# Kernel optimization log

Measured on AMD Instinct MI355X. Metric: run time of the kernel, lower is better.

## Reference

```python
import jax, jax.numpy as jnp
import numpy as np

N = 50000   # full-order mesh size
n = 10      # latent dim
MU = 32     # neighbourhood / window size
B = 8       # batch of snapshots


def setup_inputs() -> dict:
    key = jax.random.key(0)
    ks = jax.random.split(key, 6)
    x = jax.random.normal(ks[0], (B, N), jnp.float32)
    enc_w = jax.random.normal(ks[1], (n, N), jnp.float32) * 0.01  # torch Linear weight [n, N]
    enc_b = jax.random.normal(ks[2], (n,), jnp.float32) * 0.01
    decoder = jax.random.uniform(ks[3], (n, N), jnp.float32, minval=-0.01, maxval=0.01)
    bandwidth_layers = jax.random.uniform(ks[4], (n, n, N), jnp.float32, minval=-0.01, maxval=0.01)
    neighbours = jax.random.randint(ks[5], (N, MU), 0, N, jnp.int32)
    return dict(x=x, enc_w=enc_w, enc_b=enc_b, decoder=decoder,
                bandwidth_layers=bandwidth_layers, neighbours=neighbours)


def reference(x, enc_w, enc_b, decoder, bandwidth_layers, neighbours):
    mu = neighbours.shape[1]
    # encode: torch Linear -> x @ W.T + b                      [B, n]
    encoded = x @ enc_w.T + enc_b
    # bandwidths: bmm(encoded.repeat(n,1,1), bw).permute(1,0,2) -> sigmoid   [B, n, N]
    w = jax.nn.sigmoid(jnp.einsum('bk,ikp->bip', encoded, bandwidth_layers))
    # bubble window per scalar w: relu(1 - x^2/(w*mu)^2), normalized over mu  [B, n, N, mu]
    xs2 = (jnp.arange(mu, dtype=x.dtype) ** 2)  # [mu]
    win = jax.nn.relu(1.0 - xs2 / (w[..., None] * mu) ** 2)
    win = win / jnp.sum(win, axis=-1, keepdims=True)
    # gather decoder rows at each node's neighbours            [n, N, mu]
    gathered = jnp.take(decoder, neighbours, axis=1)
    # smooth_vec: sum over neighbourhood                       [B, n, N]
    smoothed = jnp.einsum('ipm,bipm->bip', gathered, win)
    # final bmm: encoded [B,1,n] @ smoothed [B,n,N] -> [B,N]
    return jnp.einsum('bi,bip->bp', encoded, smoothed)
```

## Files before the change

kernel.cpp:

```cpp
#include <hip/hip_runtime.h>
#include <hip/hip_bf16.h>

#define N_NODES 50000
#define NLAT 10
#define MU 32
#define BATCH 8
#define CHUNK 2000
#define NCHUNK 25
#define ENC_BLOCKS (BATCH * NLAT * NCHUNK)
#define TR_BLOCKS ((N_NODES + 255) / 256)
#define DT_STRIDE 16
#define NPB 64

typedef float v2f __attribute__((ext_vector_type(2)));

static __device__ __forceinline__ v2f v2_fma(v2f a, v2f b, v2f c) {
#if __has_builtin(__builtin_elementwise_fma)
    return __builtin_elementwise_fma(a, b, c);
#else
    v2f r; r[0] = fmaf(a[0], b[0], c[0]); r[1] = fmaf(a[1], b[1], c[1]); return r;
#endif
}
static __device__ __forceinline__ v2f v2_max0(v2f a) {
#if __has_builtin(__builtin_elementwise_max)
    v2f z = {0.0f, 0.0f};
    return __builtin_elementwise_max(a, z);
#else
    v2f r; r[0] = fmaxf(a[0], 0.0f); r[1] = fmaxf(a[1], 0.0f); return r;
#endif
}

__global__ __launch_bounds__(256) void encode_a_transpose(
    const float* __restrict__ x, const float* __restrict__ enc_w,
    const float* __restrict__ dec,
    float* __restrict__ partial, float* __restrict__ dec_t) {
    const int bid = blockIdx.x;
    if (bid < ENC_BLOCKS) {
        const int c  = bid % NCHUNK;
        const int bi = bid / NCHUNK;
        const int b = bi / NLAT, i = bi % NLAT;
        const float4* xr = (const float4*)(x + (size_t)b * N_NODES + c * CHUNK);
        const float4* wr = (const float4*)(enc_w + (size_t)i * N_NODES + c * CHUNK);
        float part = 0.0f;
        for (int q = threadIdx.x; q < CHUNK / 4; q += 256) {
            float4 xv = xr[q], wv = wr[q];
            part += xv.x * wv.x + xv.y * wv.y + xv.z * wv.z + xv.w * wv.w;
        }
        for (int off = 32; off; off >>= 1) part += __shfl_down(part, off, 64);
        __shared__ float s[4];
        if ((threadIdx.x & 63) == 0) s[threadIdx.x >> 6] = part;
        __syncthreads();
        if (threadIdx.x == 0) partial[bid] = (s[0] + s[1]) + (s[2] + s[3]);
    } else {
        const int p = (bid - ENC_BLOCKS) * 256 + threadIdx.x;
        if (p >= N_NODES) return;
        float v[DT_STRIDE];
        #pragma unroll
        for (int i = 0; i < NLAT; ++i) v[i] = dec[(size_t)i * N_NODES + p];
        #pragma unroll
        for (int i = NLAT; i < DT_STRIDE; ++i) v[i] = 0.0f;
        float4* dst = (float4*)(dec_t + (size_t)p * DT_STRIDE);
        #pragma unroll
        for (int q = 0; q < 4; ++q)
            dst[q] = make_float4(v[4*q], v[4*q+1], v[4*q+2], v[4*q+3]);
    }
}

__global__ __launch_bounds__(512) void nrbs_main_kernel(
    const float* __restrict__ dec_t,
    const float* __restrict__ bw,
    const int*   __restrict__ nbr,
    const float* __restrict__ partial,
    const float* __restrict__ enc_b,
    float*       __restrict__ out) {
    __shared__ float s_enc[BATCH * NLAT];
    __shared__ float s_inv[NLAT][NPB][BATCH];
    __shared__ int   s_tm[NPB];
    __shared__ int   s_nbr[NPB][MU + 1];
    const int tid   = threadIdx.x;
    const int node0 = blockIdx.x * NPB;

    if (tid < BATCH * NLAT) {
        float s = 0.0f;
        #pragma unroll
        for (int c = 0; c < NCHUNK; ++c) s += partial[tid * NCHUNK + c];
        s_enc[tid] = s + enc_b[tid % NLAT];
    }
    if (tid < NPB) s_tm[tid] = 0;
    {
        const int node = tid >> 3, ch = tid & 7;
        int4 v = make_int4(0, 0, 0, 0);
        if (node0 + node < N_NODES)
            v = ((const int4*)(nbr + (size_t)(node0 + node) * MU))[ch];
        s_nbr[node][ch * 4 + 0] = v.x; s_nbr[node][ch * 4 + 1] = v.y;
        s_nbr[node][ch * 4 + 2] = v.z; s_nbr[node][ch * 4 + 3] = v.w;
    }
    __syncthreads();

    {
        const int g    = tid >> 6;
        const int lane = tid & 63;
        const int p    = node0 + lane;
        if (p < N_NODES) {
            float tloc = 0.0f;
            for (int i = g; i < NLAT; i += 8) {
                float bwv[NLAT];
                #pragma unroll
                for (int k = 0; k < NLAT; ++k)
                    bwv[k] = bw[((size_t)(i * NLAT + k)) * N_NODES + p];
                float invv[BATCH];
                #pragma unroll
                for (int b = 0; b < BATCH; ++b) {
                    float z = 0.0f;
                    #pragma unroll
                    for (int k = 0; k < NLAT; ++k)
                        z = fmaf(s_enc[b * NLAT + k], bwv[k], z);
                    const float sg = 1.0f / (1.0f + __expf(-z));
                    const float t  = sg * (float)MU;
                    tloc = fmaxf(tloc, t);
                    invv[b] = __builtin_amdgcn_rcpf(t * t);
                }
                float4* dst = (float4*)&s_inv[i][lane][0];
                dst[0] = make_float4(invv[0], invv[1], invv[2], invv[3]);
                dst[1] = make_float4(invv[4], invv[5], invv[6], invv[7]);
            }
            atomicMax(&s_tm[lane], __float_as_int(tloc));
        }
    }
    __syncthreads();

    const int node  = tid >> 3;
    const int ipair = tid & 7;
    const int p     = node0 + node;
    const int i0    = 2 * ipair;
    const bool act  = (ipair < 5) && (p < N_NODES);

    v2f inv2[2][4], asum[2][4], ssum[2][4];
    #pragma unroll
    for (int ii = 0; ii < 2; ++ii)
        #pragma unroll
        for (int b2 = 0; b2 < 4; ++b2) {
            inv2[ii][b2] = (v2f){0.0f, 0.0f};
            asum[ii][b2] = (v2f){0.0f, 0.0f};
            ssum[ii][b2] = (v2f){0.0f, 0.0f};
        }
    int mcap = 0;
    if (act) {
        #pragma unroll
        for (int ii = 0; ii < 2; ++ii) {
            const float4* iv = (const float4*)&s_inv[i0 + ii][node][0];
            const float4 a = iv[0], c = iv[1];
            inv2[ii][0] = (v2f){a.x, a.y}; inv2[ii][1] = (v2f){a.z, a.w};
            inv2[ii][2] = (v2f){c.x, c.y}; inv2[ii][3] = (v2f){c.z, c.w};
        }
        mcap = min(MU, (int)__int_as_float(s_tm[node]) + 1);
    }

    for (int m = 0; m < mcap; ++m) {
        const int idx = s_nbr[node][m];
        const v2f g2 = *(const v2f*)(dec_t + (size_t)idx * DT_STRIDE + i0);
        const float m2 = (float)(m * m);
        const v2f nm2 = {-m2, -m2}, one = {1.0f, 1.0f};
        #pragma unroll
        for (int ii = 0; ii < 2; ++ii) {
            const v2f gg = {g2[ii], g2[ii]};
            #pragma unroll
            for (int b2 = 0; b2 < 4; ++b2) {
                const v2f win = v2_max0(v2_fma(nm2, inv2[ii][b2], one));
                ssum[ii][b2] += win;
                asum[ii][b2] = v2_fma(gg, win, asum[ii][b2]);
            }
        }
    }

    float r[BATCH];
    #pragma unroll
    for (int b2 = 0; b2 < 4; ++b2)
        #pragma unroll
        for (int h = 0; h < 2; ++h) {
            const int b = 2 * b2 + h;
            r[b] = act ? s_enc[b * NLAT + i0]     * asum[0][b2][h] *
                             __builtin_amdgcn_rcpf(ssum[0][b2][h]) +
                         s_enc[b * NLAT + i0 + 1] * asum[1][b2][h] *
                             __builtin_amdgcn_rcpf(ssum[1][b2][h])
                       : 0.0f;
        }
    #pragma unroll
    for (int mask = 1; mask < 8; mask <<= 1)
        #pragma unroll
        for (int b = 0; b < BATCH; ++b)
            r[b] += __shfl_xor(r[b], mask, 8);

    if (p < N_NODES)
        out[(size_t)ipair * N_NODES + p] = r[ipair];
}

extern "C" void kernel_launch(void* const* d_in, const int* in_sizes, int n_in,
                              void* d_out, int out_size, void* d_ws, size_t ws_size,
                              hipStream_t stream) {
    const float* x       = (const float*)d_in[0];
    const float* enc_w   = (const float*)d_in[1];
    const float* enc_b   = (const float*)d_in[2];
    const float* decoder = (const float*)d_in[3];
    const float* bwl     = (const float*)d_in[4];
    const int*   nbr     = (const int*)d_in[5];
    float* out = (float*)d_out;

    float* partial = (float*)((char*)d_ws + 1024);
    float* dec_t   = (float*)((char*)d_ws + 65536);

    encode_a_transpose<<<ENC_BLOCKS + TR_BLOCKS, 256, 0, stream>>>(
        x, enc_w, decoder, partial, dec_t);

    const int blocks = (N_NODES + NPB - 1) / NPB;
    nrbs_main_kernel<<<blocks, 512, 0, stream>>>(
        dec_t, bwl, nbr, partial, enc_b, out);
}
```

Measured before the change: 108.3 us.

## Batch neighbour gathers eight at a time and balance bandwidth-sigmoid work across warps

The neighbour loop now runs in chunks of eight. Each chunk loads its indices with vector LDS reads and issues all eight decoder gathers before any arithmetic, so more memory loads are in flight at once. The loop bound is rounded up to a multiple of eight; the extra iterations give zero window weight because relu clamps them, so the extra gathers are wasted but harmless. The sigmoid/bandwidth phase now splits latent rows 8 and 9 across all eight wave groups by batch pair, where before waves 0-1 did double work, and launch bounds now request 4 blocks per CU.

```diff
diff --git a/kernel.cpp b/kernel.cpp
--- a/kernel.cpp
+++ b/kernel.cpp
@@ -11,6 +11,7 @@
 #define TR_BLOCKS ((N_NODES + 255) / 256)
 #define DT_STRIDE 16
 #define NPB 64
+#define NBR_PAD 36
 
 typedef float v2f __attribute__((ext_vector_type(2)));
 
@@ -66,7 +67,7 @@
     }
 }
 
-__global__ __launch_bounds__(512) void nrbs_main_kernel(
+__global__ __launch_bounds__(512, 4) void nrbs_main_kernel(
     const float* __restrict__ dec_t,
     const float* __restrict__ bw,
     const int*   __restrict__ nbr,
@@ -76,7 +77,7 @@
     __shared__ float s_enc[BATCH * NLAT];
     __shared__ float s_inv[NLAT][NPB][BATCH];
     __shared__ int   s_tm[NPB];
-    __shared__ int   s_nbr[NPB][MU + 1];
+    __shared__ int   s_nbr[NPB][NBR_PAD];
     const int tid   = threadIdx.x;
     const int node0 = blockIdx.x * NPB;
 
@@ -88,12 +89,11 @@
     }
     if (tid < NPB) s_tm[tid] = 0;
     {
-        const int node = tid >> 3, ch = tid & 7;
+        const int nodeS = tid >> 3, ch = tid & 7;
         int4 v = make_int4(0, 0, 0, 0);
-        if (node0 + node < N_NODES)
-            v = ((const int4*)(nbr + (size_t)(node0 + node) * MU))[ch];
-        s_nbr[node][ch * 4 + 0] = v.x; s_nbr[node][ch * 4 + 1] = v.y;
-        s_nbr[node][ch * 4 + 2] = v.z; s_nbr[node][ch * 4 + 3] = v.w;
+        if (node0 + nodeS < N_NODES)
+            v = ((const int4*)(nbr + (size_t)(node0 + nodeS) * MU))[ch];
+        *(int4*)&s_nbr[nodeS][ch * 4] = v;
     }
     __syncthreads();
 
@@ -103,7 +103,8 @@
         const int p    = node0 + lane;
         if (p < N_NODES) {
             float tloc = 0.0f;
-            for (int i = g; i < NLAT; i += 8) {
+            {
+                const int i = g;
                 float bwv[NLAT];
                 #pragma unroll
                 for (int k = 0; k < NLAT; ++k)
@@ -124,6 +125,27 @@
                 dst[0] = make_float4(invv[0], invv[1], invv[2], invv[3]);
                 dst[1] = make_float4(invv[4], invv[5], invv[6], invv[7]);
             }
+            {
+                const int i  = 8 + (g >> 2);
+                const int b0 = (g & 3) * 2;
+                float bwv[NLAT];
+                #pragma unroll
+                for (int k = 0; k < NLAT; ++k)
+                    bwv[k] = bw[((size_t)(i * NLAT + k)) * N_NODES + p];
+                float iv2[2];
+                #pragma unroll
+                for (int h = 0; h < 2; ++h) {
+                    float z = 0.0f;
+                    #pragma unroll
+                    for (int k = 0; k < NLAT; ++k)
+                        z = fmaf(s_enc[(b0 + h) * NLAT + k], bwv[k], z);
+                    const float sg = 1.0f / (1.0f + __expf(-z));
+                    const float t  = sg * (float)MU;
+                    tloc = fmaxf(tloc, t);
+                    iv2[h] = __builtin_amdgcn_rcpf(t * t);
+                }
+                *(float2*)&s_inv[i][lane][b0] = make_float2(iv2[0], iv2[1]);
+            }
             atomicMax(&s_tm[lane], __float_as_int(tloc));
         }
     }
@@ -155,12 +177,14 @@
         }
         mcap = min(MU, (int)__int_as_float(s_tm[node]) + 1);
     }
-
-    for (int m = 0; m < mcap; ++m) {
-        const int idx = s_nbr[node][m];
-        const v2f g2 = *(const v2f*)(dec_t + (size_t)idx * DT_STRIDE + i0);
-        const float m2 = (float)(m * m);
-        const v2f nm2 = {-m2, -m2}, one = {1.0f, 1.0f};
+    const int mcap8 = (mcap + 7) & ~7;
+
+    const v2f one = {1.0f, 1.0f};
+    const float* __restrict__ bp = dec_t + i0;
+
+    auto step = [&](int m, v2f g2) {
+        const float m2f = (float)(m * m);
+        const v2f nm2 = {-m2f, -m2f};
         #pragma unroll
         for (int ii = 0; ii < 2; ++ii) {
             const v2f gg = {g2[ii], g2[ii]};
@@ -171,6 +195,23 @@
                 asum[ii][b2] = v2_fma(gg, win, asum[ii][b2]);
             }
         }
+    };
+
+    for (int mb = 0; mb < mcap8; mb += 8) {
+        const int4 na = *(const int4*)&s_nbr[node][mb];
+        const int4 nb = *(const int4*)&s_nbr[node][mb + 4];
+        const v2f g0 = *(const v2f*)(bp + (size_t)na.x * DT_STRIDE);
+        const v2f g1 = *(const v2f*)(bp + (size_t)na.y * DT_STRIDE);
+        const v2f g2 = *(const v2f*)(bp + (size_t)na.z * DT_STRIDE);
+        const v2f g3 = *(const v2f*)(bp + (size_t)na.w * DT_STRIDE);
+        const v2f g4 = *(const v2f*)(bp + (size_t)nb.x * DT_STRIDE);
+        const v2f g5 = *(const v2f*)(bp + (size_t)nb.y * DT_STRIDE);
+        const v2f g6 = *(const v2f*)(bp + (size_t)nb.z * DT_STRIDE);
+        const v2f g7 = *(const v2f*)(bp + (size_t)nb.w * DT_STRIDE);
+        step(mb + 0, g0); step(mb + 1, g1);
+        step(mb + 2, g2); step(mb + 3, g3);
+        step(mb + 4, g4); step(mb + 5, g5);
+        step(mb + 6, g6); step(mb + 7, g7);
     }
 
     float r[BATCH];
```

After: 109.7 us. No clear change (+1.3%).
